# Kernel tuning notes

Hardware: AMD Instinct MI355X
Metric: run time of the kernel (lower is better)

Reference implementation:

```python
import jax, jax.numpy as jnp
import numpy as np

B, T, C, NH = 4, 2048, 1024, 16
HD = C // NH  # head dim = 64


def setup_inputs() -> dict:
    key = jax.random.key(0)
    k1, k2, k3 = jax.random.split(key, 3)
    x = jax.random.normal(k1, (B, T, C), dtype=jnp.float32)
    w_attn = jax.random.normal(k2, (C, 3 * C), dtype=jnp.float32) * (1.0 / np.sqrt(C))
    b_attn = jnp.zeros((3 * C,), dtype=jnp.float32)
    w_proj = jax.random.normal(k3, (C, C), dtype=jnp.float32) * (1.0 / np.sqrt(C))
    b_proj = jnp.zeros((C,), dtype=jnp.float32)
    return {"x": x, "w_attn": w_attn, "b_attn": b_attn, "w_proj": w_proj, "b_proj": b_proj}


def reference(x, w_attn, b_attn, w_proj, b_proj):
    Bx, Tx, Cx = x.shape
    # fused QKV projection
    qkv = x @ w_attn + b_attn              # [B, T, 3C]
    q, k, v = jnp.split(qkv, 3, axis=-1)   # each [B, T, C]
    # split heads: [B, NH, T, HD]
    q = q.reshape(Bx, Tx, NH, HD).transpose(0, 2, 1, 3)
    k = k.reshape(Bx, Tx, NH, HD).transpose(0, 2, 1, 3)
    v = v.reshape(Bx, Tx, NH, HD).transpose(0, 2, 1, 3)
    scale = 1.0 / np.sqrt(HD)
    att = jnp.einsum('bhqd,bhkd->bhqk', q, k) * scale  # [B, NH, T, T]
    causal = jnp.tril(jnp.ones((Tx, Tx), dtype=bool))
    att = jnp.where(causal[None, None], att, -jnp.inf)
    att = jax.nn.softmax(att, axis=-1)
    y = jnp.einsum('bhqk,bhkd->bhqd', att, v)           # [B, NH, T, HD]
    y = y.transpose(0, 2, 1, 3).reshape(Bx, Tx, Cx)
    return y @ w_proj + b_proj
```

## Files before the change

kernel.cpp:

```cpp
#include <hip/hip_runtime.h>
#include <hip/hip_bf16.h>

#define B_SZ 4
#define T_SZ 2048
#define C_SZ 1024
#define NH_SZ 16
#define HD_SZ 64
#define M_SZ (B_SZ * T_SZ)

typedef __bf16 bf16x8 __attribute__((ext_vector_type(8)));
typedef __bf16 bf16x4 __attribute__((ext_vector_type(4)));
typedef float f32x4 __attribute__((ext_vector_type(4)));

__device__ __forceinline__ void async_ld16(__hip_bfloat16* lds, const __hip_bfloat16* g) {
  __builtin_amdgcn_global_load_lds(
      (const __attribute__((address_space(1))) void*)g,
      (__attribute__((address_space(3))) void*)lds, 16, 0, 0);
}

__device__ __forceinline__ void bar() {
  asm volatile("" ::: "memory");
  __builtin_amdgcn_s_barrier();
  asm volatile("" ::: "memory");
}

__device__ __forceinline__ bf16x8 frag32(const __hip_bfloat16* base, int row, int q) {
  const int byte = (row << 6) + (((q ^ (row >> 1)) & 3) << 4);
  return *(const bf16x8*)((const char*)base + byte);
}

__device__ __forceinline__ uint32_t pk2(float lo, float hi) {
  uint32_t r;
  asm("v_cvt_pk_bf16_f32 %0, %1, %2" : "=v"(r) : "v"(lo), "v"(hi));
  return r;
}

__global__ __launch_bounds__(256) void conv_bf16_kernel(
    const float* __restrict__ X, __hip_bfloat16* __restrict__ Y) {
  const int i = (blockIdx.x * 256 + threadIdx.x) * 4;
  float4 v = *(const float4*)&X[i];
  union { bf16x4 v; __hip_bfloat16 h[4]; } o;
  o.h[0] = __float2bfloat16(v.x); o.h[1] = __float2bfloat16(v.y);
  o.h[2] = __float2bfloat16(v.z); o.h[3] = __float2bfloat16(v.w);
  *(bf16x4*)&Y[i] = o.v;
}

template <int KD, int ND>
__global__ __launch_bounds__(256) void transpose_conv_kernel(
    const float* __restrict__ W, __hip_bfloat16* __restrict__ Wt) {
  __shared__ float sT[32][33];
  const int n0 = blockIdx.x * 32, k0 = blockIdx.y * 32;
  const int tid = threadIdx.x;
  {
    const int r = tid >> 3, c = (tid & 7) * 4;
    float4 v = *(const float4*)&W[(size_t)(k0 + r) * ND + n0 + c];
    sT[r][c] = v.x; sT[r][c + 1] = v.y; sT[r][c + 2] = v.z; sT[r][c + 3] = v.w;
  }
  __syncthreads();
  {
    const int n = tid >> 3, kq = (tid & 7) * 4;
    union { bf16x4 v; __hip_bfloat16 h[4]; } o;
#pragma unroll
    for (int j = 0; j < 4; ++j) o.h[j] = __float2bfloat16(sT[kq + j][n]);
    *(bf16x4*)&Wt[(size_t)(n0 + n) * KD + k0 + kq] = o.v;
  }
}


#define Q_PRESCALE 0.18033688011112042f

__global__ __launch_bounds__(512, 2) void gemm_tri256_qk(
    const __hip_bfloat16* __restrict__ A, const __hip_bfloat16* __restrict__ Bt,
    const float* __restrict__ bias,
    __hip_bfloat16* __restrict__ qR, __hip_bfloat16* __restrict__ kR) {
  __shared__ __align__(16) __hip_bfloat16 sA[3][256 * 32];
  __shared__ __align__(16) __hip_bfloat16 sB[3][256 * 32];

  const int tid = threadIdx.x;
  const int wave = tid >> 6, lane = tid & 63;
  const int quad = lane >> 4, l16 = lane & 15;
  const int wm = wave >> 2, wn = wave & 3;

  const int xcd = (int)blockIdx.x & 7, lb = (int)blockIdx.x >> 3;
  const int bm = (xcd * 4 + (lb >> 3)) * 256;
  const int bn = (lb & 7) * 256;

  const int srow = tid >> 2;
  const int scol = 8 * ((tid & 3) ^ ((tid >> 3) & 3));
  const int sdst = tid * 8;
  const __hip_bfloat16* gA = A + (size_t)(bm + srow) * C_SZ + scol;
  const __hip_bfloat16* gB = Bt + (size_t)(bn + srow) * C_SZ + scol;

  f32x4 acc[8][4];
#pragma unroll
  for (int m = 0; m < 8; ++m)
#pragma unroll
    for (int n = 0; n < 4; ++n) acc[m][n] = (f32x4){0.f, 0.f, 0.f, 0.f};

#define STG256(buf, kt)                                                         \
  do {                                                                          \
    async_ld16(&sA[buf][sdst], gA + (kt) * 32);                                 \
    async_ld16(&sA[buf][4096 + sdst], gA + (size_t)128 * C_SZ + (kt) * 32);     \
    async_ld16(&sB[buf][sdst], gB + (kt) * 32);                                 \
    async_ld16(&sB[buf][4096 + sdst], gB + (size_t)128 * C_SZ + (kt) * 32);     \
  } while (0)

  STG256(0, 0);
  STG256(1, 1);
  asm volatile("s_waitcnt vmcnt(4)" ::: "memory");
  bar();

  constexpr int NT = C_SZ / 32;
  int cur = 0;
  for (int kt = 0; kt < NT; ++kt) {
    const int stg = cur == 0 ? 2 : cur - 1;
    if (kt + 2 < NT) STG256(stg, kt + 2);

    const __hip_bfloat16* ab = sA[cur];
    const __hip_bfloat16* bb = sB[cur];
    bf16x8 af[8], bfr[4];
#pragma unroll
    for (int mq = 0; mq < 8; ++mq) af[mq] = frag32(ab, wm * 128 + mq * 16 + l16, quad);
#pragma unroll
    for (int nq = 0; nq < 4; ++nq) bfr[nq] = frag32(bb, wn * 64 + nq * 16 + l16, quad);
#pragma unroll
    for (int mq = 0; mq < 8; ++mq)
#pragma unroll
      for (int nq = 0; nq < 4; ++nq)
        acc[mq][nq] = __builtin_amdgcn_mfma_f32_16x16x32_bf16(af[mq], bfr[nq], acc[mq][nq], 0, 0, 0);

    if (kt + 1 < NT) {
      if (kt + 2 < NT) asm volatile("s_waitcnt vmcnt(4)" ::: "memory");
      else             asm volatile("s_waitcnt vmcnt(0)" ::: "memory");
      bar();
    }
    cur = cur == 2 ? 0 : cur + 1;
  }
#undef STG256

  float bv[4];
#pragma unroll
  for (int nq = 0; nq < 4; ++nq) bv[nq] = bias[bn + wn * 64 + nq * 16 + l16];
  const bool isQ = bn < C_SZ;
#pragma unroll
  for (int mq = 0; mq < 8; ++mq)
#pragma unroll
    for (int nq = 0; nq < 4; ++nq) {
      const int col = bn + wn * 64 + nq * 16 + l16;
      const int hh = (col >> 6) & 15, d = col & 63;
#pragma unroll
      for (int r = 0; r < 4; ++r) {
        const int row = bm + wm * 128 + mq * 16 + quad * 4 + r;
        const int bb_ = row >> 11, t = row & 2047;
        const size_t idx = ((size_t)(bb_ * 16 + hh) * T_SZ + t) * HD_SZ + d;
        const float val = acc[mq][nq][r] + bv[nq];
        if (isQ) qR[idx] = __float2bfloat16(val * Q_PRESCALE);
        else     kR[idx] = __float2bfloat16(val);
      }
    }
}

template <int MODE>
__global__ __launch_bounds__(256, 3) void gemm_tri128(
    const __hip_bfloat16* __restrict__ A, const __hip_bfloat16* __restrict__ Bt,
    const float* __restrict__ bias, float* __restrict__ Cf,
    __hip_bfloat16* __restrict__ vT) {
  __shared__ __align__(16) __hip_bfloat16 sA[3][128 * 32];
  __shared__ __align__(16) __hip_bfloat16 sB[3][128 * 32];

  const int tid = threadIdx.x;
  const int wave = tid >> 6, lane = tid & 63;
  const int quad = lane >> 4, l16 = lane & 15;
  const int rw = (wave & 1) * 64, cw = (wave >> 1) * 64;

  const int xcd = (int)blockIdx.x & 7, lb = (int)blockIdx.x >> 3;
  const int bm = (xcd * 8 + (lb >> 3)) * 128;
  const int bn = (lb & 7) * 128;

  const int srow = tid >> 2;
  const int scol = 8 * ((tid & 3) ^ ((tid >> 3) & 3));
  const int sdst = tid * 8;
  const __hip_bfloat16* gA = A + (size_t)(bm + srow) * C_SZ + scol;
  const __hip_bfloat16* gB = Bt + (size_t)(bn + srow) * C_SZ + scol;

  f32x4 acc[4][4];
#pragma unroll
  for (int i = 0; i < 4; ++i)
#pragma unroll
    for (int j = 0; j < 4; ++j) acc[i][j] = (f32x4){0.f, 0.f, 0.f, 0.f};

#define STG128(buf, kt)                                                        \
  do {                                                                         \
    async_ld16(&sA[buf][sdst], gA + (kt) * 32);                                \
    async_ld16(&sA[buf][2048 + sdst], gA + (size_t)64 * C_SZ + (kt) * 32);     \
    async_ld16(&sB[buf][sdst], gB + (kt) * 32);                                \
    async_ld16(&sB[buf][2048 + sdst], gB + (size_t)64 * C_SZ + (kt) * 32);     \
  } while (0)

  STG128(0, 0);
  STG128(1, 1);
  asm volatile("s_waitcnt vmcnt(4)" ::: "memory");
  bar();

  constexpr int NT = C_SZ / 32;
  int cur = 0;
  for (int kt = 0; kt < NT; ++kt) {
    const int stg = cur == 0 ? 2 : cur - 1;
    if (kt + 2 < NT) STG128(stg, kt + 2);

    const __hip_bfloat16* ab = sA[cur];
    const __hip_bfloat16* bb = sB[cur];
    bf16x8 af[4], bfr[4];
#pragma unroll
    for (int mq = 0; mq < 4; ++mq) af[mq] = frag32(ab, rw + mq * 16 + l16, quad);
#pragma unroll
    for (int nq = 0; nq < 4; ++nq) bfr[nq] = frag32(bb, cw + nq * 16 + l16, quad);
#pragma unroll
    for (int mq = 0; mq < 4; ++mq)
#pragma unroll
      for (int nq = 0; nq < 4; ++nq)
        acc[mq][nq] = __builtin_amdgcn_mfma_f32_16x16x32_bf16(af[mq], bfr[nq], acc[mq][nq], 0, 0, 0);

    if (kt + 1 < NT) {
      if (kt + 2 < NT) asm volatile("s_waitcnt vmcnt(4)" ::: "memory");
      else             asm volatile("s_waitcnt vmcnt(0)" ::: "memory");
      bar();
    }
    cur = cur == 2 ? 0 : cur + 1;
  }
#undef STG128

  float bv[4];
#pragma unroll
  for (int nq = 0; nq < 4; ++nq) bv[nq] = bias[bn + cw + nq * 16 + l16];
#pragma unroll
  for (int mq = 0; mq < 4; ++mq)
#pragma unroll
    for (int nq = 0; nq < 4; ++nq) {
      const int col = bn + cw + nq * 16 + l16;
#pragma unroll
      for (int r = 0; r < 4; ++r) {
        const int row = bm + rw + mq * 16 + quad * 4 + r;
        const float val = acc[mq][nq][r] + bv[nq];
        if (MODE == 0) {
          const int bb_ = row >> 11, t = row & 2047;
          const int hh = col >> 6, d = col & 63;
          vT[((size_t)(bb_ * 16 + hh) * HD_SZ + d) * T_SZ + t] = __float2bfloat16(val);
        } else {
          Cf[(size_t)row * C_SZ + col] = val;
        }
      }
    }
}

#define ATT_ST 72

__device__ __forceinline__ void p_exchange(
    const f32x4& s0, const f32x4& s1, const f32x4& s2, const f32x4& s3,
    bool uSel, bool cSel, int srcE, int srcO, bf16x8& A0v, bf16x8& A1v) {
  uint32_t pk[4][2];
  pk[0][0] = pk2(s0[0], s0[1]); pk[0][1] = pk2(s0[2], s0[3]);
  pk[1][0] = pk2(s1[0], s1[1]); pk[1][1] = pk2(s1[2], s1[3]);
  pk[2][0] = pk2(s2[0], s2[1]); pk[2][1] = pk2(s2[2], s2[3]);
  pk[3][0] = pk2(s3[0], s3[1]); pk[3][1] = pk2(s3[2], s3[3]);

  uint32_t g0 = (uint32_t)__shfl((int)(uSel ? pk[1][0] : pk[0][0]), srcE, 64);
  uint32_t g1 = (uint32_t)__shfl((int)(uSel ? pk[0][0] : pk[1][0]), srcO, 64);
  uint32_t g2 = (uint32_t)__shfl((int)(uSel ? pk[3][0] : pk[2][0]), srcE, 64);
  uint32_t g3 = (uint32_t)__shfl((int)(uSel ? pk[2][0] : pk[3][0]), srcO, 64);
  uint32_t g4 = (uint32_t)__shfl((int)(uSel ? pk[1][1] : pk[0][1]), srcE, 64);
  uint32_t g5 = (uint32_t)__shfl((int)(uSel ? pk[0][1] : pk[1][1]), srcO, 64);
  uint32_t g6 = (uint32_t)__shfl((int)(uSel ? pk[3][1] : pk[2][1]), srcE, 64);
  uint32_t g7 = (uint32_t)__shfl((int)(uSel ? pk[2][1] : pk[3][1]), srcO, 64);

  union PU { uint32_t d[4]; bf16x8 v; } A0, A1;
  A0.d[0] = cSel ? g1 : g0;  A0.d[1] = cSel ? g5 : g4;
  A0.d[2] = cSel ? g0 : g1;  A0.d[3] = cSel ? g4 : g5;
  A1.d[0] = cSel ? g3 : g2;  A1.d[1] = cSel ? g7 : g6;
  A1.d[2] = cSel ? g2 : g3;  A1.d[3] = cSel ? g6 : g7;
  A0v = A0.v;
  A1v = A1.v;
}

__global__ __launch_bounds__(256, 3) void attn_mfma_kernel(
    const __hip_bfloat16* __restrict__ qR, const __hip_bfloat16* __restrict__ kR,
    const __hip_bfloat16* __restrict__ vT, __hip_bfloat16* __restrict__ y) {
  __shared__ __align__(16) __hip_bfloat16 sQ[128][ATT_ST];
  __shared__ __align__(16) __hip_bfloat16 sK[64][ATT_ST];
  __shared__ __align__(16) __hip_bfloat16 sVt[64][ATT_ST];

  const int bh = blockIdx.x;
  const int tile = (int)gridDim.y - 1 - blockIdx.y;
  const int t0 = tile * 128;
  const int tid = threadIdx.x;
  const int wave = tid >> 6, lane = tid & 63;
  const int quad = lane >> 4, l16 = lane & 15;
  const int wrowQ = wave * 32;

  const __hip_bfloat16* qb = qR + (size_t)bh * T_SZ * HD_SZ;
  const __hip_bfloat16* kb = kR + (size_t)bh * T_SZ * HD_SZ;
  const __hip_bfloat16* vb = vT + (size_t)bh * HD_SZ * T_SZ;

  const int sr = tid >> 2, sc = (tid & 3) * 16;

  const bool uSel = (quad & 1) != 0;
  const bool cSel = (quad >> 1) != 0;
  const int srcE = l16 + 32 * (quad & 1) + 16 * (quad >> 1);
  const int srcO = srcE ^ 16;

  {
    const __hip_bfloat16* src = qb + (size_t)t0 * HD_SZ + tid * 16;
    *(float4*)&sQ[sr][sc] = *(const float4*)src;
    *(float4*)&sQ[sr][sc + 8] = *(const float4*)(src + 8);
    const __hip_bfloat16* src2 = src + 64 * HD_SZ;
    *(float4*)&sQ[64 + sr][sc] = *(const float4*)src2;
    *(float4*)&sQ[64 + sr][sc + 8] = *(const float4*)(src2 + 8);
  }

  float4 krg0, krg1, vrg0, vrg1;
  {
    const __hip_bfloat16* ks = kb + tid * 16;
    krg0 = *(const float4*)ks;
    krg1 = *(const float4*)(ks + 8);
    const __hip_bfloat16* vs = vb + (size_t)sr * T_SZ + sc;
    vrg0 = *(const float4*)vs;
    vrg1 = *(const float4*)(vs + 8);
  }

  __syncthreads();
  bf16x8 qa[2][2];
#pragma unroll
  for (int g = 0; g < 2; ++g) {
    qa[g][0] = *(const bf16x8*)&sQ[wrowQ + g * 16 + l16][quad * 8];
    qa[g][1] = *(const bf16x8*)&sQ[wrowQ + g * 16 + l16][32 + quad * 8];
  }

  float lacc0 = 0.f, lacc1 = 0.f;
  f32x4 o[2][4];
#pragma unroll
  for (int g = 0; g < 2; ++g)
#pragma unroll
    for (int nn = 0; nn < 4; ++nn) o[g][nn] = (f32x4){0.f, 0.f, 0.f, 0.f};

  const int jmax = t0 + 64;
  for (int j0 = 0; j0 <= jmax; j0 += 64) {
    *(float4*)&sK[sr][sc] = krg0;
    *(float4*)&sK[sr][sc + 8] = krg1;
    *(float4*)&sVt[sr][sc] = vrg0;
    *(float4*)&sVt[sr][sc + 8] = vrg1;
    if (j0 + 64 <= jmax) {
      const __hip_bfloat16* ks = kb + (size_t)(j0 + 64) * HD_SZ + tid * 16;
      krg0 = *(const float4*)ks;
      krg1 = *(const float4*)(ks + 8);
      const __hip_bfloat16* vs = vb + (size_t)sr * T_SZ + j0 + 64 + sc;
      vrg0 = *(const float4*)vs;
      vrg1 = *(const float4*)(vs + 8);
    }
    __syncthreads();

    f32x4 s0[4], s1[4];
    __builtin_amdgcn_s_setprio(1);
#pragma unroll
    for (int sub = 0; sub < 4; ++sub) {
      bf16x8 kf0 = *(const bf16x8*)&sK[sub * 16 + l16][quad * 8];
      bf16x8 kf1 = *(const bf16x8*)&sK[sub * 16 + l16][32 + quad * 8];
      s0[sub] = (f32x4){0.f, 0.f, 0.f, 0.f};
      s0[sub] = __builtin_amdgcn_mfma_f32_16x16x32_bf16(kf0, qa[0][0], s0[sub], 0, 0, 0);
      s0[sub] = __builtin_amdgcn_mfma_f32_16x16x32_bf16(kf1, qa[0][1], s0[sub], 0, 0, 0);
      s1[sub] = (f32x4){0.f, 0.f, 0.f, 0.f};
      s1[sub] = __builtin_amdgcn_mfma_f32_16x16x32_bf16(kf0, qa[1][0], s1[sub], 0, 0, 0);
      s1[sub] = __builtin_amdgcn_mfma_f32_16x16x32_bf16(kf1, qa[1][1], s1[sub], 0, 0, 0);
    }
    __builtin_amdgcn_s_setprio(0);

    {
      const int qb0 = t0 + wrowQ;
      if (j0 + 63 > qb0) {
        const int qrow = qb0 + l16;
#pragma unroll
        for (int sub = 0; sub < 4; ++sub)
#pragma unroll
          for (int r = 0; r < 4; ++r)
            if (j0 + sub * 16 + quad * 4 + r > qrow) s0[sub][r] = -1e30f;
      }
      const int qb1 = qb0 + 16;
      if (j0 + 63 > qb1) {
        const int qrow = qb1 + l16;
#pragma unroll
        for (int sub = 0; sub < 4; ++sub)
#pragma unroll
          for (int r = 0; r < 4; ++r)
            if (j0 + sub * 16 + quad * 4 + r > qrow) s1[sub][r] = -1e30f;
      }
    }

#pragma unroll
    for (int sub = 0; sub < 4; ++sub)
#pragma unroll
      for (int r = 0; r < 4; ++r) {
        s0[sub][r] = __builtin_amdgcn_exp2f(s0[sub][r]);
        s1[sub][r] = __builtin_amdgcn_exp2f(s1[sub][r]);
      }
#pragma unroll
    for (int sub = 0; sub < 4; ++sub) {
      lacc0 += (s0[sub][0] + s0[sub][1]) + (s0[sub][2] + s0[sub][3]);
      lacc1 += (s1[sub][0] + s1[sub][1]) + (s1[sub][2] + s1[sub][3]);
    }

    bf16x8 A0g0, A1g0, A0g1, A1g1;
    p_exchange(s0[0], s0[1], s0[2], s0[3], uSel, cSel, srcE, srcO, A0g0, A1g0);
    p_exchange(s1[0], s1[1], s1[2], s1[3], uSel, cSel, srcE, srcO, A0g1, A1g1);

    __builtin_amdgcn_s_setprio(1);
#pragma unroll
    for (int nn = 0; nn < 4; ++nn) {
      bf16x8 vf0 = *(const bf16x8*)&sVt[nn * 16 + l16][quad * 8];
      bf16x8 vf1 = *(const bf16x8*)&sVt[nn * 16 + l16][32 + quad * 8];
      o[0][nn] = __builtin_amdgcn_mfma_f32_16x16x32_bf16(A0g0, vf0, o[0][nn], 0, 0, 0);
      o[0][nn] = __builtin_amdgcn_mfma_f32_16x16x32_bf16(A1g0, vf1, o[0][nn], 0, 0, 0);
      o[1][nn] = __builtin_amdgcn_mfma_f32_16x16x32_bf16(A0g1, vf0, o[1][nn], 0, 0, 0);
      o[1][nn] = __builtin_amdgcn_mfma_f32_16x16x32_bf16(A1g1, vf1, o[1][nn], 0, 0, 0);
    }
    __builtin_amdgcn_s_setprio(0);

    if (j0 < jmax) __syncthreads();
  }

  lacc0 += __shfl_xor(lacc0, 16);
  lacc0 += __shfl_xor(lacc0, 32);
  lacc1 += __shfl_xor(lacc1, 16);
  lacc1 += __shfl_xor(lacc1, 32);
  float inv[2][4];
#pragma unroll
  for (int r = 0; r < 4; ++r) {
    inv[0][r] = 1.0f / __shfl(lacc0, (lane & 48) + quad * 4 + r, 64);
    inv[1][r] = 1.0f / __shfl(lacc1, (lane & 48) + quad * 4 + r, 64);
  }

  const int b = bh >> 4, h = bh & 15;
#pragma unroll
  for (int g = 0; g < 2; ++g)
#pragma unroll
    for (int nn = 0; nn < 4; ++nn)
#pragma unroll
      for (int r = 0; r < 4; ++r) {
        const int t = t0 + wrowQ + g * 16 + quad * 4 + r;
        y[((size_t)b * T_SZ + t) * C_SZ + h * HD_SZ + nn * 16 + l16] =
            __float2bfloat16(o[g][nn][r] * inv[g][r]);
      }
}

extern "C" void kernel_launch(void* const* d_in, const int* in_sizes, int n_in,
                              void* d_out, int out_size, void* d_ws, size_t ws_size,
                              hipStream_t stream) {
  const float* x      = (const float*)d_in[0];
  const float* w_attn = (const float*)d_in[1];
  const float* b_attn = (const float*)d_in[2];
  const float* w_proj = (const float*)d_in[3];
  const float* b_proj = (const float*)d_in[4];
  float* out = (float*)d_out;

  __hip_bfloat16* xb  = (__hip_bfloat16*)d_ws;
  __hip_bfloat16* waT = xb + (size_t)M_SZ * C_SZ;
  __hip_bfloat16* wpT = waT + (size_t)3 * C_SZ * C_SZ;
  __hip_bfloat16* qR  = wpT + (size_t)C_SZ * C_SZ;
  __hip_bfloat16* kR  = qR + (size_t)M_SZ * C_SZ;
  __hip_bfloat16* vT  = kR + (size_t)M_SZ * C_SZ;
  __hip_bfloat16* yb  = xb;

  conv_bf16_kernel<<<(M_SZ * C_SZ) / (256 * 4), 256, 0, stream>>>(x, xb);
  transpose_conv_kernel<C_SZ, 3 * C_SZ><<<dim3(96, 32), 256, 0, stream>>>(w_attn, waT);
  transpose_conv_kernel<C_SZ, C_SZ><<<dim3(32, 32), 256, 0, stream>>>(w_proj, wpT);

  gemm_tri256_qk<<<dim3(256), 512, 0, stream>>>(xb, waT, b_attn, qR, kR);

  gemm_tri128<0><<<dim3(512), 256, 0, stream>>>(
      xb, waT + (size_t)2 * C_SZ * C_SZ, b_attn + 2 * C_SZ, nullptr, vT);

  attn_mfma_kernel<<<dim3(B_SZ * NH_SZ, T_SZ / 128), 256, 0, stream>>>(qR, kR, vT, yb);

  gemm_tri128<1><<<dim3(512), 256, 0, stream>>>(
      (const __hip_bfloat16*)yb, wpT, b_proj, out, nullptr);
}
```

Baseline: 249.8 us.

## Shrink QK GEMM tile to 256x128 and swizzle attention LDS tiles

The Q/K projection GEMM moves from 256x256 tiles on 256 blocks to 256x128 tiles on 512 blocks. It uses 8 waves in a 4x2 arrangement, and launch bounds now allow 4 blocks per CU, aiming for better occupancy and load balance. The attention kernel replaces its padded LDS rows (stride 72) with a dense 64-wide layout and an XOR swizzle, intended to avoid bank conflicts while using less LDS. In exchange, each QK block reuses less data from LDS, so it does more global loads per FLOP.

Result: faster. 242.4 us (-3.0%).

```diff
diff --git a/kernel.cpp b/kernel.cpp
--- a/kernel.cpp
+++ b/kernel.cpp
@@ -28,6 +28,8 @@
   const int byte = (row << 6) + (((q ^ (row >> 1)) & 3) << 4);
   return *(const bf16x8*)((const char*)base + byte);
 }
+
+#define SWZ(row, cb) (((row) << 7) + ((cb) ^ (((row) & 7) << 4)))
 
 __device__ __forceinline__ uint32_t pk2(float lo, float hi) {
   uint32_t r;
@@ -69,21 +71,21 @@
 
 #define Q_PRESCALE 0.18033688011112042f
 
-__global__ __launch_bounds__(512, 2) void gemm_tri256_qk(
+__global__ __launch_bounds__(512, 4) void gemm_qk_ring(
     const __hip_bfloat16* __restrict__ A, const __hip_bfloat16* __restrict__ Bt,
     const float* __restrict__ bias,
     __hip_bfloat16* __restrict__ qR, __hip_bfloat16* __restrict__ kR) {
   __shared__ __align__(16) __hip_bfloat16 sA[3][256 * 32];
-  __shared__ __align__(16) __hip_bfloat16 sB[3][256 * 32];
+  __shared__ __align__(16) __hip_bfloat16 sB[3][128 * 32];
 
   const int tid = threadIdx.x;
   const int wave = tid >> 6, lane = tid & 63;
   const int quad = lane >> 4, l16 = lane & 15;
-  const int wm = wave >> 2, wn = wave & 3;
+  const int wm = wave >> 1, wn = wave & 1;
 
   const int xcd = (int)blockIdx.x & 7, lb = (int)blockIdx.x >> 3;
-  const int bm = (xcd * 4 + (lb >> 3)) * 256;
-  const int bn = (lb & 7) * 256;
+  const int bm = (xcd * 4 + (lb >> 4)) * 256;
+  const int bn = (lb & 15) * 128;
 
   const int srow = tid >> 2;
   const int scol = 8 * ((tid & 3) ^ ((tid >> 3) & 3));
@@ -91,66 +93,65 @@
   const __hip_bfloat16* gA = A + (size_t)(bm + srow) * C_SZ + scol;
   const __hip_bfloat16* gB = Bt + (size_t)(bn + srow) * C_SZ + scol;
 
-  f32x4 acc[8][4];
-#pragma unroll
-  for (int m = 0; m < 8; ++m)
-#pragma unroll
-    for (int n = 0; n < 4; ++n) acc[m][n] = (f32x4){0.f, 0.f, 0.f, 0.f};
-
-#define STG256(buf, kt)                                                         \
-  do {                                                                          \
-    async_ld16(&sA[buf][sdst], gA + (kt) * 32);                                 \
-    async_ld16(&sA[buf][4096 + sdst], gA + (size_t)128 * C_SZ + (kt) * 32);     \
-    async_ld16(&sB[buf][sdst], gB + (kt) * 32);                                 \
-    async_ld16(&sB[buf][4096 + sdst], gB + (size_t)128 * C_SZ + (kt) * 32);     \
+  f32x4 acc[4][4];
+#pragma unroll
+  for (int i = 0; i < 4; ++i)
+#pragma unroll
+    for (int j = 0; j < 4; ++j) acc[i][j] = (f32x4){0.f, 0.f, 0.f, 0.f};
+
+#define STGQK(buf, kt)                                                         \
+  do {                                                                         \
+    async_ld16(&sA[buf][sdst], gA + (kt) * 32);                                \
+    async_ld16(&sA[buf][4096 + sdst], gA + (size_t)128 * C_SZ + (kt) * 32);    \
+    async_ld16(&sB[buf][sdst], gB + (kt) * 32);                                \
   } while (0)
 
-  STG256(0, 0);
-  STG256(1, 1);
-  asm volatile("s_waitcnt vmcnt(4)" ::: "memory");
+  STGQK(0, 0);
+  STGQK(1, 1);
+  asm volatile("s_waitcnt vmcnt(3)" ::: "memory");
   bar();
 
   constexpr int NT = C_SZ / 32;
   int cur = 0;
   for (int kt = 0; kt < NT; ++kt) {
     const int stg = cur == 0 ? 2 : cur - 1;
-    if (kt + 2 < NT) STG256(stg, kt + 2);
+    if (kt + 2 < NT) STGQK(stg, kt + 2);
 
     const __hip_bfloat16* ab = sA[cur];
     const __hip_bfloat16* bb = sB[cur];
-    bf16x8 af[8], bfr[4];
-#pragma unroll
-    for (int mq = 0; mq < 8; ++mq) af[mq] = frag32(ab, wm * 128 + mq * 16 + l16, quad);
+    bf16x8 af[4], bfr[4];
+#pragma unroll
+    for (int mq = 0; mq < 4; ++mq) af[mq] = frag32(ab, wm * 64 + mq * 16 + l16, quad);
 #pragma unroll
     for (int nq = 0; nq < 4; ++nq) bfr[nq] = frag32(bb, wn * 64 + nq * 16 + l16, quad);
 #pragma unroll
-    for (int mq = 0; mq < 8; ++mq)
+    for (int mq = 0; mq < 4; ++mq)
 #pragma unroll
       for (int nq = 0; nq < 4; ++nq)
         acc[mq][nq] = __builtin_amdgcn_mfma_f32_16x16x32_bf16(af[mq], bfr[nq], acc[mq][nq], 0, 0, 0);
 
     if (kt + 1 < NT) {
-      if (kt + 2 < NT) asm volatile("s_waitcnt vmcnt(4)" ::: "memory");
+      if (kt + 2 < NT) asm volatile("s_waitcnt vmcnt(3)" ::: "memory");
       else             asm volatile("s_waitcnt vmcnt(0)" ::: "memory");
       bar();
     }
     cur = cur == 2 ? 0 : cur + 1;
   }
-#undef STG256
+#undef STGQK
 
   float bv[4];
 #pragma unroll
   for (int nq = 0; nq < 4; ++nq) bv[nq] = bias[bn + wn * 64 + nq * 16 + l16];
   const bool isQ = bn < C_SZ;
 #pragma unroll
-  for (int mq = 0; mq < 8; ++mq)
+  for (int mq = 0; mq < 4; ++mq)
 #pragma unroll
     for (int nq = 0; nq < 4; ++nq) {
       const int col = bn + wn * 64 + nq * 16 + l16;
       const int hh = (col >> 6) & 15, d = col & 63;
 #pragma unroll
       for (int r = 0; r < 4; ++r) {
-        const int row = bm + wm * 128 + mq * 16 + quad * 4 + r;
+        const int row = bm + wm * 64 + mq * 16 + quad * 4 + r;
         const int bb_ = row >> 11, t = row & 2047;
         const size_t idx = ((size_t)(bb_ * 16 + hh) * T_SZ + t) * HD_SZ + d;
         const float val = acc[mq][nq][r] + bv[nq];
@@ -253,7 +254,6 @@
     }
 }
 
-#define ATT_ST 72
 
 __device__ __forceinline__ void p_exchange(
     const f32x4& s0, const f32x4& s1, const f32x4& s2, const f32x4& s3,
@@ -285,9 +285,9 @@
 __global__ __launch_bounds__(256, 3) void attn_mfma_kernel(
     const __hip_bfloat16* __restrict__ qR, const __hip_bfloat16* __restrict__ kR,
     const __hip_bfloat16* __restrict__ vT, __hip_bfloat16* __restrict__ y) {
-  __shared__ __align__(16) __hip_bfloat16 sQ[128][ATT_ST];
-  __shared__ __align__(16) __hip_bfloat16 sK[64][ATT_ST];
-  __shared__ __align__(16) __hip_bfloat16 sVt[64][ATT_ST];
+  __shared__ __align__(16) __hip_bfloat16 sQ[128 * 64];
+  __shared__ __align__(16) __hip_bfloat16 sK[64 * 64];
+  __shared__ __align__(16) __hip_bfloat16 sVt[64 * 64];
 
   const int bh = blockIdx.x;
   const int tile = (int)gridDim.y - 1 - blockIdx.y;
@@ -301,7 +301,9 @@
   const __hip_bfloat16* kb = kR + (size_t)bh * T_SZ * HD_SZ;
   const __hip_bfloat16* vb = vT + (size_t)bh * HD_SZ * T_SZ;
 
-  const int sr = tid >> 2, sc = (tid & 3) * 16;
+  const int sr = tid >> 2;
+  const int cb = 32 * (tid & 3);
+  const int scE = (tid & 3) * 16;
 
   const bool uSel = (quad & 1) != 0;
   const bool cSel = (quad >> 1) != 0;
@@ -310,11 +312,11 @@
 
   {
     const __hip_bfloat16* src = qb + (size_t)t0 * HD_SZ + tid * 16;
-    *(float4*)&sQ[sr][sc] = *(const float4*)src;
-    *(float4*)&sQ[sr][sc + 8] = *(const float4*)(src + 8);
+    *(float4*)((char*)sQ + SWZ(sr, cb)) = *(const float4*)src;
+    *(float4*)((char*)sQ + SWZ(sr, cb + 16)) = *(const float4*)(src + 8);
     const __hip_bfloat16* src2 = src + 64 * HD_SZ;
-    *(float4*)&sQ[64 + sr][sc] = *(const float4*)src2;
-    *(float4*)&sQ[64 + sr][sc + 8] = *(const float4*)(src2 + 8);
+    *(float4*)((char*)sQ + SWZ(64 + sr, cb)) = *(const float4*)src2;
+    *(float4*)((char*)sQ + SWZ(64 + sr, cb + 16)) = *(const float4*)(src2 + 8);
   }
 
   float4 krg0, krg1, vrg0, vrg1;
@@ -322,7 +324,7 @@
     const __hip_bfloat16* ks = kb + tid * 16;
     krg0 = *(const float4*)ks;
     krg1 = *(const float4*)(ks + 8);
-    const __hip_bfloat16* vs = vb + (size_t)sr * T_SZ + sc;
+    const __hip_bfloat16* vs = vb + (size_t)sr * T_SZ + scE;
     vrg0 = *(const float4*)vs;
     vrg1 = *(const float4*)(vs + 8);
   }
@@ -331,8 +333,9 @@
   bf16x8 qa[2][2];
 #pragma unroll
   for (int g = 0; g < 2; ++g) {
-    qa[g][0] = *(const bf16x8*)&sQ[wrowQ + g * 16 + l16][quad * 8];
-    qa[g][1] = *(const bf16x8*)&sQ[wrowQ + g * 16 + l16][32 + quad * 8];
+    const int qr = wrowQ + g * 16 + l16;
+    qa[g][0] = *(const bf16x8*)((const char*)sQ + SWZ(qr, quad * 16));
+    qa[g][1] = *(const bf16x8*)((const char*)sQ + SWZ(qr, 64 + quad * 16));
   }
 
   float lacc0 = 0.f, lacc1 = 0.f;
@@ -344,15 +347,15 @@
 
   const int jmax = t0 + 64;
   for (int j0 = 0; j0 <= jmax; j0 += 64) {
-    *(float4*)&sK[sr][sc] = krg0;
-    *(float4*)&sK[sr][sc + 8] = krg1;
-    *(float4*)&sVt[sr][sc] = vrg0;
-    *(float4*)&sVt[sr][sc + 8] = vrg1;
+    *(float4*)((char*)sK + SWZ(sr, cb)) = krg0;
+    *(float4*)((char*)sK + SWZ(sr, cb + 16)) = krg1;
+    *(float4*)((char*)sVt + SWZ(sr, cb)) = vrg0;
+    *(float4*)((char*)sVt + SWZ(sr, cb + 16)) = vrg1;
     if (j0 + 64 <= jmax) {
       const __hip_bfloat16* ks = kb + (size_t)(j0 + 64) * HD_SZ + tid * 16;
       krg0 = *(const float4*)ks;
       krg1 = *(const float4*)(ks + 8);
-      const __hip_bfloat16* vs = vb + (size_t)sr * T_SZ + j0 + 64 + sc;
+      const __hip_bfloat16* vs = vb + (size_t)sr * T_SZ + j0 + 64 + scE;
       vrg0 = *(const float4*)vs;
       vrg1 = *(const float4*)(vs + 8);
     }
@@ -362,8 +365,9 @@
     __builtin_amdgcn_s_setprio(1);
 #pragma unroll
     for (int sub = 0; sub < 4; ++sub) {
-      bf16x8 kf0 = *(const bf16x8*)&sK[sub * 16 + l16][quad * 8];
-      bf16x8 kf1 = *(const bf16x8*)&sK[sub * 16 + l16][32 + quad * 8];
+      const int kr = sub * 16 + l16;
+      bf16x8 kf0 = *(const bf16x8*)((const char*)sK + SWZ(kr, quad * 16));
+      bf16x8 kf1 = *(const bf16x8*)((const char*)sK + SWZ(kr, 64 + quad * 16));
       s0[sub] = (f32x4){0.f, 0.f, 0.f, 0.f};
       s0[sub] = __builtin_amdgcn_mfma_f32_16x16x32_bf16(kf0, qa[0][0], s0[sub], 0, 0, 0);
       s0[sub] = __builtin_amdgcn_mfma_f32_16x16x32_bf16(kf1, qa[0][1], s0[sub], 0, 0, 0);
@@ -414,8 +418,9 @@
     __builtin_amdgcn_s_setprio(1);
 #pragma unroll
     for (int nn = 0; nn < 4; ++nn) {
-      bf16x8 vf0 = *(const bf16x8*)&sVt[nn * 16 + l16][quad * 8];
-      bf16x8 vf1 = *(const bf16x8*)&sVt[nn * 16 + l16][32 + quad * 8];
+      const int vr = nn * 16 + l16;
+      bf16x8 vf0 = *(const bf16x8*)((const char*)sVt + SWZ(vr, quad * 16));
+      bf16x8 vf1 = *(const bf16x8*)((const char*)sVt + SWZ(vr, 64 + quad * 16));
       o[0][nn] = __builtin_amdgcn_mfma_f32_16x16x32_bf16(A0g0, vf0, o[0][nn], 0, 0, 0);
       o[0][nn] = __builtin_amdgcn_mfma_f32_16x16x32_bf16(A1g0, vf1, o[0][nn], 0, 0, 0);
       o[1][nn] = __builtin_amdgcn_mfma_f32_16x16x32_bf16(A0g1, vf0, o[1][nn], 0, 0, 0);
@@ -472,7 +477,7 @@
   transpose_conv_kernel<C_SZ, 3 * C_SZ><<<dim3(96, 32), 256, 0, stream>>>(w_attn, waT);
   transpose_conv_kernel<C_SZ, C_SZ><<<dim3(32, 32), 256, 0, stream>>>(w_proj, wpT);
 
-  gemm_tri256_qk<<<dim3(256), 512, 0, stream>>>(xb, waT, b_attn, qR, kR);
+  gemm_qk_ring<<<dim3(512), 512, 0, stream>>>(xb, waT, b_attn, qR, kR);
 
   gemm_tri128<0><<<dim3(512), 256, 0, stream>>>(
       xb, waT + (size_t)2 * C_SZ * C_SZ, b_attn + 2 * C_SZ, nullptr, vT);
```
